# Optimization experiments

Measured on AMD Instinct MI355X. Metric: run time of the kernel, lower is better.

Reference implementation:

```python
import jax, jax.numpy as jnp
import numpy as np

EMBED = 1024
HEADS = 16
HEAD_DIM = EMBED // HEADS
MAX_REL = 16


def setup_inputs() -> dict:
    key = jax.random.key(0)
    ks = jax.random.split(key, 8)
    s = 0.02
    x = jax.random.normal(ks[0], (4, 2048, EMBED), dtype=jnp.float32)
    Wq = jax.random.normal(ks[1], (EMBED, EMBED), dtype=jnp.float32) * s
    bq = jnp.zeros((EMBED,), dtype=jnp.float32)
    Wk = jax.random.normal(ks[2], (EMBED, EMBED), dtype=jnp.float32) * s
    bk = jnp.zeros((EMBED,), dtype=jnp.float32)
    Wv = jax.random.normal(ks[3], (EMBED, EMBED), dtype=jnp.float32) * s
    bv = jnp.zeros((EMBED,), dtype=jnp.float32)
    rel_bias = jax.random.normal(ks[4], (2 * MAX_REL + 1, HEADS), dtype=jnp.float32) * s
    return {"x": x, "Wq": Wq, "bq": bq, "Wk": Wk, "bk": bk, "Wv": Wv, "bv": bv, "rel_bias": rel_bias}


def reference(x, Wq, bq, Wk, bk, Wv, bv, rel_bias):
    B, S, _ = x.shape
    # projections (Linear: x @ W + b, with W stored [in, out])
    q = (x @ Wq + bq).reshape(B, S, HEADS, HEAD_DIM).transpose(0, 2, 1, 3)  # [B,H,S,D]
    k = (x @ Wk + bk).reshape(B, S, HEADS, HEAD_DIM).transpose(0, 2, 1, 3)
    v = (x @ Wv + bv).reshape(B, S, HEADS, HEAD_DIM).transpose(0, 2, 1, 3)
    scores = jnp.einsum('bhqd,bhkd->bhqk', q, k) / jnp.sqrt(jnp.float32(HEAD_DIM))
    pos = jnp.arange(S)
    rel = jnp.clip(pos[None, :] - pos[:, None], -MAX_REL, MAX_REL) + MAX_REL  # [S,S]
    bias = rel_bias[rel]                      # [S,S,H]
    scores = scores + bias.transpose(2, 0, 1)[None]  # [B,H,S,S]
    probs = jax.nn.softmax(scores, axis=-1)
    # dropout is identity in eval mode
    out = jnp.einsum('bhqk,bhkd->bhqd', probs, v)
    return out.transpose(0, 2, 1, 3).reshape(B, S, EMBED)
```

## Files before the change

kernel.cpp:

```cpp
#include <hip/hip_runtime.h>

#define EMBED 1024
#define HEADS 16
#define HDIM  64
#define SEQ   2048
#define BATCH 4
#define MTOT  (BATCH*SEQ)

typedef __attribute__((ext_vector_type(8)))  short short8;
typedef __attribute__((ext_vector_type(4)))  float f32x4;
typedef __attribute__((ext_vector_type(16))) float f32x16;

#define GLOAD_LDS16(g, l) \
  __builtin_amdgcn_global_load_lds((const __attribute__((address_space(1))) void*)(g), \
                                   (__attribute__((address_space(3))) void*)(l), 16, 0, 0)

__device__ inline unsigned short f2bf(float f) {
  union { float f; unsigned u; } v; v.f = f;
  unsigned r = v.u + 0x7FFF + ((v.u >> 16) & 1);
  return (unsigned short)(r >> 16);
}

__device__ inline unsigned cvtpk(float lo, float hi) {
  unsigned r;
  asm("v_cvt_pk_bf16_f32 %0, %1, %2" : "=v"(r) : "v"(lo), "v"(hi));
  return r;
}

__device__ inline float vexp2(float x) {
  float r;
  asm("v_exp_f32 %0, %1" : "=v"(r) : "v"(x));
  return r;
}

#define PLSWAP(a, b) asm("v_permlane32_swap_b32 %0, %1" : "+v"(a), "+v"(b))

__device__ inline short8 mk8(unsigned w0, unsigned w1, unsigned w2, unsigned w3) {
  union { unsigned u[4]; short8 s; } x;
  x.u[0] = w0; x.u[1] = w1; x.u[2] = w2; x.u[3] = w3;
  return x.s;
}

__global__ void cvt_x(const float* __restrict__ x, unsigned short* __restrict__ xb) {
  int i = (blockIdx.x * blockDim.x + threadIdx.x) * 8;
  f32x4 a = *(const f32x4*)(x + i);
  f32x4 b = *(const f32x4*)(x + i + 4);
  unsigned short o[8];
  o[0]=f2bf(a[0]); o[1]=f2bf(a[1]); o[2]=f2bf(a[2]); o[3]=f2bf(a[3]);
  o[4]=f2bf(b[0]); o[5]=f2bf(b[1]); o[6]=f2bf(b[2]); o[7]=f2bf(b[3]);
  *(short8*)(xb + i) = *(short8*)o;
}

__global__ void transpose_w(const float* __restrict__ Wq, const float* __restrict__ Wk,
                            const float* __restrict__ Wv, unsigned short* __restrict__ Wtb) {
  __shared__ float tile[32][33];
  int wsel = blockIdx.z;
  const float* W = wsel == 0 ? Wq : (wsel == 1 ? Wk : Wv);
  int k0 = blockIdx.x * 32, n0 = blockIdx.y * 32;
  int tx = threadIdx.x & 31, ty = threadIdx.x >> 5;
  for (int i = 0; i < 4; ++i)
    tile[ty + i*8][tx] = W[(k0 + ty + i*8) * EMBED + n0 + tx];
  __syncthreads();
  unsigned short* o = Wtb + wsel * EMBED * EMBED;
  for (int i = 0; i < 4; ++i)
    o[(n0 + ty + i*8) * EMBED + k0 + tx] = f2bf(tile[tx][ty + i*8]);
}

__global__ __launch_bounds__(256)
void qkv_gemm(const unsigned short* __restrict__ xb, const unsigned short* __restrict__ Wtb,
              const float* __restrict__ bq, const float* __restrict__ bk, const float* __restrict__ bv,
              unsigned short* __restrict__ Qb, unsigned short* __restrict__ Kb,
              unsigned short* __restrict__ Vt) {
  __shared__ unsigned short As[128 * 72];
  __shared__ unsigned short Bs[128 * 72];
  int wsel = blockIdx.z;
  int m0 = blockIdx.x * 128, n0 = blockIdx.y * 128;
  int t = threadIdx.x, lane = t & 63, wave = t >> 6;
  int wr = wave >> 1, wc = wave & 1;
  int lr = lane & 15, lg = lane >> 4;
  const unsigned short* Wt = Wtb + wsel * (EMBED * EMBED);
  const float* bias = wsel == 0 ? bq : (wsel == 1 ? bk : bv);

  f32x4 acc[4][4] = {};

  for (int kt = 0; kt < EMBED / 64; ++kt) {
    int k0 = kt * 64;
    for (int i = 0; i < 4; ++i) {
      int c = i * 256 + t;
      int row = c >> 3, col8 = c & 7;
      short8 va = *(const short8*)(xb + (m0 + row) * EMBED + k0 + col8 * 8);
      short8 vb = *(const short8*)(Wt + (n0 + row) * EMBED + k0 + col8 * 8);
      *(short8*)(As + row * 72 + col8 * 8) = va;
      *(short8*)(Bs + row * 72 + col8 * 8) = vb;
    }
    __syncthreads();
    for (int kk = 0; kk < 2; ++kk) {
      short8 af[4], bfr[4];
      for (int mf = 0; mf < 4; ++mf)
        af[mf] = *(const short8*)(As + (wr * 64 + mf * 16 + lr) * 72 + kk * 32 + lg * 8);
      for (int nf = 0; nf < 4; ++nf)
        bfr[nf] = *(const short8*)(Bs + (wc * 64 + nf * 16 + lr) * 72 + kk * 32 + lg * 8);
      for (int mf = 0; mf < 4; ++mf)
        for (int nf = 0; nf < 4; ++nf)
          acc[mf][nf] = __builtin_amdgcn_mfma_f32_16x16x32_bf16(af[mf], bfr[nf], acc[mf][nf], 0, 0, 0);
    }
    __syncthreads();
  }

  const float SCLQ = 0.125f * 1.44269504088896340736f;
  for (int nf = 0; nf < 4; ++nf) {
    int n = n0 + wc * 64 + nf * 16 + lr;
    float bval = bias[n];
    int h = n >> 6, d = n & 63;
    for (int mf = 0; mf < 4; ++mf) {
      for (int r = 0; r < 4; ++r) {
        int m = m0 + wr * 64 + mf * 16 + lg * 4 + r;
        int b = m >> 11, s = m & 2047;
        float oval = acc[mf][nf][r] + bval;
        if (wsel == 0) oval *= SCLQ;
        unsigned short bfv = f2bf(oval);
        if (wsel == 0)      Qb[((b * HEADS + h) * SEQ + s) * HDIM + d] = bfv;
        else if (wsel == 1) Kb[((b * HEADS + h) * SEQ + s) * HDIM + d] = bfv;
        else                Vt[((b * HEADS + h) * HDIM + d) * SEQ + s] = bfv;
      }
    }
  }
}

__global__ __launch_bounds__(256)
void attn(const unsigned short* __restrict__ Qb, const unsigned short* __restrict__ Kb,
          const unsigned short* __restrict__ Vt, const float* __restrict__ rel_bias,
          float* __restrict__ out) {
  __shared__ unsigned short KVs[16384];
  __shared__ float bias_l[33];
  __shared__ float dld[4][32];
  int bh = blockIdx.y;
  int b = bh >> 4, h = bh & 15;
  int t = threadIdx.x, lane = t & 63, wave = t >> 6;
  int l31 = lane & 31, hi = lane >> 5;
  const float LOG2E = 1.44269504088896340736f;
  if (t < 33) bias_l[t] = rel_bias[t * HEADS + h] * LOG2E;

  int qw0 = blockIdx.x * 128 + wave * 32;
  const unsigned short* Qp = Qb + (bh * SEQ + qw0) * HDIM;
  const unsigned short* Kp = Kb + bh * SEQ * HDIM;
  const unsigned short* Vp = Vt + bh * HDIM * SEQ;

  short8 qf[4];
  #pragma unroll
  for (int ks = 0; ks < 4; ++ks)
    qf[ks] = *(const short8*)(Qp + l31 * HDIM + ks * 16 + hi * 8);

  unsigned rbo[2][4];
  #pragma unroll
  for (int rs = 0; rs < 2; ++rs)
    #pragma unroll
    for (int ks = 0; ks < 4; ++ks) {
      int row = rs * 32 + l31;
      rbo[rs][ks] = (unsigned)((row << 7) + ((((ks << 1) | hi) ^ (row & 7)) << 4));
    }
  #define LDK(rs, ks, BUF) \
    (*(const short8*)((const char*)KVs + rbo[rs][ks] + (BUF) * 8192))
  #define LDVv(rs, ks, BUF) \
    (*(const short8*)((const char*)KVs + rbo[rs][ks] + 16384 + (BUF) * 8192))

  f32x16 O0 = {}, O1 = {};
  float ls0 = 0.f, ls1 = 0.f, ls2 = 0.f, ls3 = 0.f;
  int q = qw0 + l31;

  int srow0 = (wave << 4) + (lane >> 3);
  int sslot = lane & 7;

  #define STAGE(BUF, key0_)                                                          \
    for (int j = 0; j < 2; ++j) {                                                    \
      int srow = srow0 + j * 8;                                                      \
      int cs = sslot ^ (srow & 7);                                                   \
      GLOAD_LDS16(Kp + ((key0_) + srow) * HDIM + cs * 8,                             \
                  &KVs[(BUF) * 4096 + (((wave << 4) + j * 8) << 6)]);                \
      GLOAD_LDS16(Vp + srow * SEQ + (key0_) + cs * 8,                                \
                  &KVs[8192 + (BUF) * 4096 + (((wave << 4) + j * 8) << 6)]);         \
    }

  STAGE(0, 0)
  __syncthreads();
  float cbLo = bias_l[0], cbHi = bias_l[32];

  #define PROC(SACC, KOFF, BUF)  {                                                   \
    float pv[16];                                                                    \
    int kbase = key0 + (KOFF);                                                       \
    if (kbase >= qw0 + 47) {                                                         \
      _Pragma("unroll") for (int r = 0; r < 16; ++r)                                 \
        pv[r] = vexp2(SACC[r] + cbHi);                                               \
    } else if (kbase <= qw0 - 47) {                                                  \
      _Pragma("unroll") for (int r = 0; r < 16; ++r)                                 \
        pv[r] = vexp2(SACC[r] + cbLo);                                               \
    } else {                                                                         \
      _Pragma("unroll") for (int r = 0; r < 16; ++r) {                               \
        int key = kbase + (r & 3) + 8 * (r >> 2) + 4 * hi;                           \
        int rel = key - q;                                                           \
        rel = rel < -16 ? -16 : (rel > 16 ? 16 : rel);                               \
        pv[r] = vexp2(SACC[r] + bias_l[rel + 16]);                                   \
      }                                                                              \
    }                                                                                \
    ls0 += (pv[0] + pv[1]) + (pv[2] + pv[3]);                                        \
    ls1 += (pv[4] + pv[5]) + (pv[6] + pv[7]);                                        \
    ls2 += (pv[8] + pv[9]) + (pv[10] + pv[11]);                                      \
    ls3 += (pv[12] + pv[13]) + (pv[14] + pv[15]);                                    \
                       \
    unsigned a0 = cvtpk(pv[0], pv[1]),  a1 = cvtpk(pv[4], pv[5]);   PLSWAP(a0, a1);  \
    unsigned a2 = cvtpk(pv[2], pv[3]),  a3 = cvtpk(pv[6], pv[7]);   PLSWAP(a2, a3);  \
    unsigned b0 = cvtpk(pv[8], pv[9]),  b1 = cvtpk(pv[12], pv[13]); PLSWAP(b0, b1);  \
    unsigned b2 = cvtpk(pv[10], pv[11]), b3 = cvtpk(pv[14], pv[15]); PLSWAP(b2, b3); \
    short8 pa0 = mk8(a0, a2, a1, a3);                                                \
    short8 pa1 = mk8(b0, b2, b1, b3);                                                \
    O0 = __builtin_amdgcn_mfma_f32_32x32x16_bf16(pa0, LDVv(0, (KOFF)/16, BUF),     O0, 0, 0, 0); \
    O1 = __builtin_amdgcn_mfma_f32_32x32x16_bf16(pa0, LDVv(1, (KOFF)/16, BUF),     O1, 0, 0, 0); \
    O0 = __builtin_amdgcn_mfma_f32_32x32x16_bf16(pa1, LDVv(0, (KOFF)/16 + 1, BUF), O0, 0, 0, 0); \
    O1 = __builtin_amdgcn_mfma_f32_32x32x16_bf16(pa1, LDVv(1, (KOFF)/16 + 1, BUF), O1, 0, 0, 0); \
  }

  #define QKT(BUF, S0, S1)                                                           \
    f32x16 S0 = {}, S1 = {};                                                         \
    _Pragma("unroll") for (int ks = 0; ks < 4; ++ks) {                               \
      S0 = __builtin_amdgcn_mfma_f32_32x32x16_bf16(LDK(0, ks, BUF), qf[ks], S0, 0, 0, 0); \
      S1 = __builtin_amdgcn_mfma_f32_32x32x16_bf16(LDK(1, ks, BUF), qf[ks], S1, 0, 0, 0); \
    }

  for (int kbp = 0; kbp < 16; ++kbp) {
    {
      int key0 = (kbp * 2) * 64;
      STAGE(1, key0 + 64)
      QKT(0, s0, s1)
      PROC(s0, 0, 0)
      PROC(s1, 32, 0)
      __syncthreads();
    }
    {
      int key0 = (kbp * 2 + 1) * 64;
      if (kbp < 15) { STAGE(0, key0 + 64) }
      QKT(1, s0, s1)
      PROC(s0, 0, 1)
      PROC(s1, 32, 1)
      __syncthreads();
    }
  }

  float lsum = (ls0 + ls1) + (ls2 + ls3);
  float denom = lsum + __shfl_xor(lsum, 32, 64);
  if (lane < 32) dld[wave][l31] = 1.0f / denom;
  float* op = out + (b * SEQ + qw0) * EMBED + h * HDIM;
  #pragma unroll
  for (int r = 0; r < 16; ++r) {
    int ql = (r & 3) + 8 * (r >> 2) + 4 * hi;
    float inv = dld[wave][ql];
    op[ql * EMBED + l31]      = O0[r] * inv;
    op[ql * EMBED + 32 + l31] = O1[r] * inv;
  }
  #undef STAGE
  #undef LDK
  #undef LDVv
  #undef PROC
  #undef QKT
}

extern "C" void kernel_launch(void* const* d_in, const int* in_sizes, int n_in,
                              void* d_out, int out_size, void* d_ws, size_t ws_size,
                              hipStream_t stream) {
  const float* x        = (const float*)d_in[0];
  const float* Wq       = (const float*)d_in[1];
  const float* bq       = (const float*)d_in[2];
  const float* Wk       = (const float*)d_in[3];
  const float* bk       = (const float*)d_in[4];
  const float* Wv       = (const float*)d_in[5];
  const float* bv       = (const float*)d_in[6];
  const float* rel_bias = (const float*)d_in[7];
  float* out = (float*)d_out;

  char* ws = (char*)d_ws;
  unsigned short* xb  = (unsigned short*)(ws);
  unsigned short* Wtb = (unsigned short*)(ws + 16777216);
  unsigned short* Qb  = (unsigned short*)(ws + 23068672);
  unsigned short* Kb  = (unsigned short*)(ws + 39845888);
  unsigned short* Vt  = (unsigned short*)(ws + 56623104);

  cvt_x<<<MTOT * EMBED / (256 * 8), 256, 0, stream>>>(x, xb);
  transpose_w<<<dim3(32, 32, 3), 256, 0, stream>>>(Wq, Wk, Wv, Wtb);
  qkv_gemm<<<dim3(MTOT / 128, EMBED / 128, 3), 256, 0, stream>>>(xb, Wtb, bq, bk, bv, Qb, Kb, Vt);
  attn<<<dim3(SEQ / 128, BATCH * HEADS), 256, 0, stream>>>(Qb, Kb, Vt, rel_bias, out);
}
```

Baseline: 203.9 us.

## Process 64 query rows per wave to reuse staged K/V tiles

Each wave now handles two 32-row query sub-tiles instead of one, doubling the block's query tile to 256 rows and halving the attention grid. Every K/V tile staged in LDS is reused for twice as many queries, which cuts global K/V traffic and the number of staging barriers per query. In exchange each wave holds double the Q fragments and output accumulators, which raises register pressure and may lower occupancy. The grid also drops to 512 blocks, which could leave compute units underused.

```diff
diff --git a/kernel.cpp b/kernel.cpp
--- a/kernel.cpp
+++ b/kernel.cpp
@@ -133,7 +133,7 @@
           float* __restrict__ out) {
   __shared__ unsigned short KVs[16384];
   __shared__ float bias_l[33];
-  __shared__ float dld[4][32];
+  __shared__ float dld[4][2][32];
   int bh = blockIdx.y;
   int b = bh >> 4, h = bh & 15;
   int t = threadIdx.x, lane = t & 63, wave = t >> 6;
@@ -141,15 +141,17 @@
   const float LOG2E = 1.44269504088896340736f;
   if (t < 33) bias_l[t] = rel_bias[t * HEADS + h] * LOG2E;
 
-  int qw0 = blockIdx.x * 128 + wave * 32;
+  int qw0 = blockIdx.x * 256 + wave * 64;
   const unsigned short* Qp = Qb + (bh * SEQ + qw0) * HDIM;
   const unsigned short* Kp = Kb + bh * SEQ * HDIM;
   const unsigned short* Vp = Vt + bh * HDIM * SEQ;
 
-  short8 qf[4];
+  short8 qfA[4], qfB[4];
   #pragma unroll
-  for (int ks = 0; ks < 4; ++ks)
-    qf[ks] = *(const short8*)(Qp + l31 * HDIM + ks * 16 + hi * 8);
+  for (int ks = 0; ks < 4; ++ks) {
+    qfA[ks] = *(const short8*)(Qp + l31 * HDIM + ks * 16 + hi * 8);
+    qfB[ks] = *(const short8*)(Qp + (32 + l31) * HDIM + ks * 16 + hi * 8);
+  }
 
   unsigned rbo[2][4];
   #pragma unroll
@@ -164,9 +166,9 @@
   #define LDVv(rs, ks, BUF) \
     (*(const short8*)((const char*)KVs + rbo[rs][ks] + 16384 + (BUF) * 8192))
 
-  f32x16 O0 = {}, O1 = {};
-  float ls0 = 0.f, ls1 = 0.f, ls2 = 0.f, ls3 = 0.f;
-  int q = qw0 + l31;
+  f32x16 OA0 = {}, OA1 = {}, OB0 = {}, OB1 = {};
+  float lsA0 = 0.f, lsA1 = 0.f, lsB0 = 0.f, lsB1 = 0.f;
+  int qA = qw0 + l31, qB = qw0 + 32 + l31;
 
   int srow0 = (wave << 4) + (lane >> 3);
   int sslot = lane & 7;
@@ -185,27 +187,25 @@
   __syncthreads();
   float cbLo = bias_l[0], cbHi = bias_l[32];
 
-  #define PROC(SACC, KOFF, BUF)  {                                                   \
+  #define PROC(SACC, KOFF, BUF, QW, QV, LS0, LS1, OD0, OD1)  {                       \
     float pv[16];                                                                    \
     int kbase = key0 + (KOFF);                                                       \
-    if (kbase >= qw0 + 47) {                                                         \
+    if (kbase >= (QW) + 47) {                                                        \
       _Pragma("unroll") for (int r = 0; r < 16; ++r)                                 \
         pv[r] = vexp2(SACC[r] + cbHi);                                               \
-    } else if (kbase <= qw0 - 47) {                                                  \
+    } else if (kbase <= (QW) - 47) {                                                 \
       _Pragma("unroll") for (int r = 0; r < 16; ++r)                                 \
         pv[r] = vexp2(SACC[r] + cbLo);                                               \
     } else {                                                                         \
       _Pragma("unroll") for (int r = 0; r < 16; ++r) {                               \
         int key = kbase + (r & 3) + 8 * (r >> 2) + 4 * hi;                           \
-        int rel = key - q;                                                           \
+        int rel = key - (QV);                                                        \
         rel = rel < -16 ? -16 : (rel > 16 ? 16 : rel);                               \
         pv[r] = vexp2(SACC[r] + bias_l[rel + 16]);                                   \
       }                                                                              \
     }                                                                                \
-    ls0 += (pv[0] + pv[1]) + (pv[2] + pv[3]);                                        \
-    ls1 += (pv[4] + pv[5]) + (pv[6] + pv[7]);                                        \
-    ls2 += (pv[8] + pv[9]) + (pv[10] + pv[11]);                                      \
-    ls3 += (pv[12] + pv[13]) + (pv[14] + pv[15]);                                    \
+    LS0 += ((pv[0] + pv[1]) + (pv[2] + pv[3])) + ((pv[4] + pv[5]) + (pv[6] + pv[7]));\
+    LS1 += ((pv[8] + pv[9]) + (pv[10] + pv[11])) + ((pv[12] + pv[13]) + (pv[14] + pv[15]));\
                        \
     unsigned a0 = cvtpk(pv[0], pv[1]),  a1 = cvtpk(pv[4], pv[5]);   PLSWAP(a0, a1);  \
     unsigned a2 = cvtpk(pv[2], pv[3]),  a3 = cvtpk(pv[6], pv[7]);   PLSWAP(a2, a3);  \
@@ -213,54 +213,66 @@
     unsigned b2 = cvtpk(pv[10], pv[11]), b3 = cvtpk(pv[14], pv[15]); PLSWAP(b2, b3); \
     short8 pa0 = mk8(a0, a2, a1, a3);                                                \
     short8 pa1 = mk8(b0, b2, b1, b3);                                                \
-    O0 = __builtin_amdgcn_mfma_f32_32x32x16_bf16(pa0, LDVv(0, (KOFF)/16, BUF),     O0, 0, 0, 0); \
-    O1 = __builtin_amdgcn_mfma_f32_32x32x16_bf16(pa0, LDVv(1, (KOFF)/16, BUF),     O1, 0, 0, 0); \
-    O0 = __builtin_amdgcn_mfma_f32_32x32x16_bf16(pa1, LDVv(0, (KOFF)/16 + 1, BUF), O0, 0, 0, 0); \
-    O1 = __builtin_amdgcn_mfma_f32_32x32x16_bf16(pa1, LDVv(1, (KOFF)/16 + 1, BUF), O1, 0, 0, 0); \
-  }
-
-  #define QKT(BUF, S0, S1)                                                           \
+    OD0 = __builtin_amdgcn_mfma_f32_32x32x16_bf16(pa0, LDVv(0, (KOFF)/16, BUF),     OD0, 0, 0, 0); \
+    OD1 = __builtin_amdgcn_mfma_f32_32x32x16_bf16(pa0, LDVv(1, (KOFF)/16, BUF),     OD1, 0, 0, 0); \
+    OD0 = __builtin_amdgcn_mfma_f32_32x32x16_bf16(pa1, LDVv(0, (KOFF)/16 + 1, BUF), OD0, 0, 0, 0); \
+    OD1 = __builtin_amdgcn_mfma_f32_32x32x16_bf16(pa1, LDVv(1, (KOFF)/16 + 1, BUF), OD1, 0, 0, 0); \
+  }
+
+  #define QKT(BUF, QF, S0, S1)                                                       \
     f32x16 S0 = {}, S1 = {};                                                         \
     _Pragma("unroll") for (int ks = 0; ks < 4; ++ks) {                               \
-      S0 = __builtin_amdgcn_mfma_f32_32x32x16_bf16(LDK(0, ks, BUF), qf[ks], S0, 0, 0, 0); \
-      S1 = __builtin_amdgcn_mfma_f32_32x32x16_bf16(LDK(1, ks, BUF), qf[ks], S1, 0, 0, 0); \
-    }
+      S0 = __builtin_amdgcn_mfma_f32_32x32x16_bf16(LDK(0, ks, BUF), QF[ks], S0, 0, 0, 0); \
+      S1 = __builtin_amdgcn_mfma_f32_32x32x16_bf16(LDK(1, ks, BUF), QF[ks], S1, 0, 0, 0); \
+    }
+
+  #define PHASE(BUF, KEY0, DO_STAGE)  {                                              \
+    int key0 = (KEY0);                                                               \
+    if (DO_STAGE) { STAGE(BUF ^ 1, key0 + 64) }                                      \
+    {                                                                                \
+      QKT(BUF, qfA, s0, s1)                                                          \
+      PROC(s0, 0,  BUF, qw0, qA, lsA0, lsA1, OA0, OA1)                               \
+      PROC(s1, 32, BUF, qw0, qA, lsA0, lsA1, OA0, OA1)                               \
+    }                                                                                \
+    {                                                                                \
+      QKT(BUF, qfB, s0, s1)                                                          \
+      PROC(s0, 0,  BUF, qw0 + 32, qB, lsB0, lsB1, OB0, OB1)                          \
+      PROC(s1, 32, BUF, qw0 + 32, qB, lsB0, lsB1, OB0, OB1)                          \
+    }                                                                                \
+    __syncthreads();                                                                 \
+  }
 
   for (int kbp = 0; kbp < 16; ++kbp) {
-    {
-      int key0 = (kbp * 2) * 64;
-      STAGE(1, key0 + 64)
-      QKT(0, s0, s1)
-      PROC(s0, 0, 0)
-      PROC(s1, 32, 0)
-      __syncthreads();
-    }
-    {
-      int key0 = (kbp * 2 + 1) * 64;
-      if (kbp < 15) { STAGE(0, key0 + 64) }
-      QKT(1, s0, s1)
-      PROC(s0, 0, 1)
-      PROC(s1, 32, 1)
-      __syncthreads();
-    }
-  }
-
-  float lsum = (ls0 + ls1) + (ls2 + ls3);
-  float denom = lsum + __shfl_xor(lsum, 32, 64);
-  if (lane < 32) dld[wave][l31] = 1.0f / denom;
-  float* op = out + (b * SEQ + qw0) * EMBED + h * HDIM;
+    PHASE(0, (kbp * 2) * 64, 1)
+    PHASE(1, (kbp * 2 + 1) * 64, kbp < 15)
+  }
+
+  {
+    float lsum = lsA0 + lsA1;
+    float denom = lsum + __shfl_xor(lsum, 32, 64);
+    if (lane < 32) dld[wave][0][l31] = 1.0f / denom;
+    lsum = lsB0 + lsB1;
+    denom = lsum + __shfl_xor(lsum, 32, 64);
+    if (lane < 32) dld[wave][1][l31] = 1.0f / denom;
+  }
+  float* opA = out + (b * SEQ + qw0) * EMBED + h * HDIM;
+  float* opB = opA + 32 * EMBED;
   #pragma unroll
   for (int r = 0; r < 16; ++r) {
     int ql = (r & 3) + 8 * (r >> 2) + 4 * hi;
-    float inv = dld[wave][ql];
-    op[ql * EMBED + l31]      = O0[r] * inv;
-    op[ql * EMBED + 32 + l31] = O1[r] * inv;
+    float invA = dld[wave][0][ql];
+    float invB = dld[wave][1][ql];
+    opA[ql * EMBED + l31]      = OA0[r] * invA;
+    opA[ql * EMBED + 32 + l31] = OA1[r] * invA;
+    opB[ql * EMBED + l31]      = OB0[r] * invB;
+    opB[ql * EMBED + 32 + l31] = OB1[r] * invB;
   }
   #undef STAGE
   #undef LDK
   #undef LDVv
   #undef PROC
   #undef QKT
+  #undef PHASE
 }
 
 extern "C" void kernel_launch(void* const* d_in, const int* in_sizes, int n_in,
@@ -286,5 +298,5 @@
   cvt_x<<<MTOT * EMBED / (256 * 8), 256, 0, stream>>>(x, xb);
   transpose_w<<<dim3(32, 32, 3), 256, 0, stream>>>(Wq, Wk, Wv, Wtb);
   qkv_gemm<<<dim3(MTOT / 128, EMBED / 128, 3), 256, 0, stream>>>(xb, Wtb, bq, bk, bv, Qb, Kb, Vt);
-  attn<<<dim3(SEQ / 128, BATCH * HEADS), 256, 0, stream>>>(Qb, Kb, Vt, rel_bias, out);
-}
+  attn<<<dim3(SEQ / 256, BATCH * HEADS), 256, 0, stream>>>(Qb, Kb, Vt, rel_bias, out);
+}
```

Result: slower. 240.0 us (+17.7%).
